# Kernel tuning notes

Measured on AMD Instinct MI355X. Metric: run time of the kernel, lower is better.

The kernel has to match this reference:

```python
import jax, jax.numpy as jnp
import numpy as np

B, N, C = 8, 1024, 768
NH, HD = 12, 64  # num_heads, head_dim
S = 32           # spatial_size (H = W = S, N = S*S)


def _rel_pos_idx(h, w):
    # Standard Swin-style relative position index, shape (h*w, h*w)
    coords = np.stack(np.meshgrid(np.arange(h), np.arange(w), indexing='ij'))  # (2, h, w)
    coords = coords.reshape(2, -1)                                             # (2, N)
    rel = coords[:, :, None] - coords[:, None, :]                              # (2, N, N)
    rel = rel.transpose(1, 2, 0).astype(np.int64)                              # (N, N, 2)
    rel[:, :, 0] += h - 1
    rel[:, :, 1] += w - 1
    rel[:, :, 0] *= 2 * w - 1
    return rel.sum(-1).astype(np.int32)                                        # (N, N)


def setup_inputs() -> dict:
    key = jax.random.key(0)
    ks = jax.random.split(key, 7)
    lim = (1.0 / C) ** 0.5
    x = jax.random.normal(ks[0], (B, N, C), dtype=jnp.float32)
    Wq = jax.random.uniform(ks[1], (C, C), minval=-lim, maxval=lim, dtype=jnp.float32)
    bq = jax.random.uniform(ks[2], (C,), minval=-lim, maxval=lim, dtype=jnp.float32)
    Wkv = jax.random.uniform(ks[3], (2 * C, C), minval=-lim, maxval=lim, dtype=jnp.float32)
    bkv = jax.random.uniform(ks[4], (2 * C,), minval=-lim, maxval=lim, dtype=jnp.float32)
    rel_bias = jax.random.uniform(ks[5], ((2 * S - 1) * (2 * S - 1), NH), dtype=jnp.float32)
    rel_idx = jnp.asarray(_rel_pos_idx(S, S))  # (N, N) int32
    return {"x": x, "Wq": Wq, "bq": bq, "Wkv": Wkv, "bkv": bkv,
            "rel_bias": rel_bias, "rel_idx": rel_idx, "H": S, "W": S}


def reference(x, Wq, bq, Wkv, bkv, rel_bias, rel_idx, H, W):
    b, n, c = x.shape
    scale = HD ** (-0.5)
    # Q projection: (B, NH, N, HD)
    q = (x @ Wq.T + bq).reshape(b, n, NH, HD).transpose(0, 2, 1, 3) * scale
    # KV projection (reduction_factor == 1, no downsample)
    kv = (x @ Wkv.T + bkv).reshape(b, n, 2, NH, HD)
    k = kv[:, :, 0].transpose(0, 2, 1, 3)  # (B, NH, N, HD)
    v = kv[:, :, 1].transpose(0, 2, 1, 3)  # (B, NH, N, HD)
    # Attention scores + gathered relative-position bias
    attn = jnp.einsum('bhqd,bhkd->bhqk', q, k)
    bias = rel_bias[rel_idx]                # (N, N, NH) gather
    attn = attn + bias.transpose(2, 0, 1)[None]
    attn = jax.nn.softmax(attn, axis=-1)
    out = jnp.einsum('bhqk,bhkd->bhqd', attn, v)
    out = out.transpose(0, 2, 1, 3).reshape(b, n, c)
    # NOTE: original forward never applies self.proj; dropout p=0 is identity.
    return out
```

## Files before the change

### kernel.cpp

```cpp
#include <hip/hip_runtime.h>


using bf16x8 = __attribute__((ext_vector_type(8))) short;
using f32x4  = __attribute__((ext_vector_type(4))) float;
using s16x4  = __attribute__((ext_vector_type(4))) short;
using f32x4v = __attribute__((ext_vector_type(4))) float;

#define DEVINL __device__ __forceinline__

#if __has_builtin(__builtin_amdgcn_exp2f)
#define EXP2(x) __builtin_amdgcn_exp2f(x)
#else
#define EXP2(x) __expf((x) * 0.6931471805599453f)
#endif

DEVINL float b2f(short s) {
  union { unsigned u; float f; } v;
  v.u = ((unsigned)(unsigned short)s) << 16;
  return v.f;
}
DEVINL short f2b(float f) {
  union { float f; unsigned u; } v; v.f = f;
  unsigned r = v.u + 0x7fffu + ((v.u >> 16) & 1u);
  return (short)(r >> 16);
}

DEVINL int is_bf16(const unsigned* xraw) {
  int cnt = 0;
#pragma unroll
  for (int i = 0; i < 64; ++i) {
    unsigned e = (xraw[i] >> 7) & 0xffu;
    cnt += (e >= 0x60u && e <= 0xa0u) ? 1 : 0;
  }
  return cnt >= 48;
}

DEVINL void gl_lds16(const short* g, short* l) {
  __builtin_amdgcn_global_load_lds(
      (const __attribute__((address_space(1))) unsigned int*)g,
      (__attribute__((address_space(3))) unsigned int*)l, 16, 0, 0);
}

__global__ __launch_bounds__(256) void convert_kernel(
    const void* __restrict__ x, const void* __restrict__ wq,
    const void* __restrict__ bq, const void* __restrict__ wkv,
    const void* __restrict__ bkv, const void* __restrict__ rb,
    short* __restrict__ xc, short* __restrict__ wqc, short* __restrict__ bqc,
    short* __restrict__ wkvc, short* __restrict__ bkvc,
    short* __restrict__ rbc) {
  const int bf = is_bf16((const unsigned*)x);
  long t = ((long)blockIdx.x * 256 + threadIdx.x) * 4;
  const void* src; short* dst; long i;
  if (t < 6291456L)      { src = x;   dst = xc;   i = t; }
  else if (t < 6881280L) { src = wq;  dst = wqc;  i = t - 6291456L; }
  else if (t < 6882048L) { src = bq;  dst = bqc;  i = t - 6881280L; }
  else if (t < 8061696L) { src = wkv; dst = wkvc; i = t - 6882048L; }
  else if (t < 8063232L) { src = bkv; dst = bkvc; i = t - 8061696L; }
  else if (t < 8110860L) { src = rb;  dst = rbc;  i = t - 8063232L; }
  else return;
  s16x4 o;
  if (bf) {
    o = *(const s16x4*)((const short*)src + i);
  } else {
    f32x4v v = *(const f32x4v*)((const float*)src + i);
    o[0] = f2b(v[0]); o[1] = f2b(v[1]); o[2] = f2b(v[2]); o[3] = f2b(v[3]);
  }
  *(s16x4*)(dst + i) = o;
}

__global__ __launch_bounds__(256) void bias_pack_kernel(
    const int* __restrict__ rel_idx, const short* __restrict__ rel_bias,
    short* __restrict__ bias_pk) {
  int t = blockIdx.x * 256 + threadIdx.x;
  int l15 = t & 15, qq = (t >> 4) & 255, kt4 = (t >> 12) & 3, kt = t >> 14;
  int k = kt * 64 + kt4 * 16 + l15;
  union { unsigned long long u[3]; short s[12]; } row[4];
#pragma unroll
  for (int r = 0; r < 4; ++r) {
    int q = qq * 4 + r;
    int idx = rel_idx[q * 1024 + k];
    const unsigned long long* src =
        (const unsigned long long*)(rel_bias + (size_t)idx * 12);
    row[r].u[0] = src[0]; row[r].u[1] = src[1]; row[r].u[2] = src[2];
  }
#pragma unroll
  for (int hh = 0; hh < 12; ++hh) {
    s16x4 v;
    v[0] = f2b(b2f(row[0].s[hh]) * 1.44269504f);
    v[1] = f2b(b2f(row[1].s[hh]) * 1.44269504f);
    v[2] = f2b(b2f(row[2].s[hh]) * 1.44269504f);
    v[3] = f2b(b2f(row[3].s[hh]) * 1.44269504f);
    *(s16x4*)(bias_pk +
              ((((size_t)(hh * 16 + kt) * 4 + kt4) * 256 + qq) * 16 + l15) * 4) = v;
  }
}

__global__ __launch_bounds__(512, 6) void qkv_gemm_kernel(
    const short* __restrict__ x, const short* __restrict__ wq,
    const short* __restrict__ wkv, const short* __restrict__ bq,
    const short* __restrict__ bkv, short* __restrict__ qbuf,
    short* __restrict__ kbuf, short* __restrict__ vtbuf) {
  __shared__ short lds_a[8192];
  __shared__ short lds_b[8192];
  const int tid = threadIdx.x;
  const int w = tid >> 6, lane = tid & 63, quad = lane >> 4, l15 = lane & 15;
  const int bid = blockIdx.x;
  const int xcd = bid & 7, local = bid >> 3;
  const int m_tile = xcd * 8 + (local & 7), n_tile = local >> 3;
  const int m0 = m_tile * 128, n0 = n_tile * 128;
  const short* wsrc = (n0 < 768) ? (wq + (size_t)n0 * 768)
                                 : (wkv + (size_t)(n0 - 768) * 768);
  const int wm = (w & 1) * 64, wn = (w >> 1) * 32;
  const int lrow = lane >> 3;
  const int lcol = ((lane & 7) ^ lrow) * 8;
  f32x4 acc[4][2] = {};

  for (int k0 = 0; k0 < 768; k0 += 64) {
    __syncthreads();
#pragma unroll
    for (int c = 0; c < 2; ++c) {
      int r0 = (c * 8 + w) * 8;
      gl_lds16(x + (size_t)(m0 + r0 + lrow) * 768 + k0 + lcol, &lds_a[r0 * 64]);
      gl_lds16(wsrc + (size_t)(r0 + lrow) * 768 + k0 + lcol, &lds_b[r0 * 64]);
    }
    __syncthreads();
#pragma unroll
    for (int ks = 0; ks < 2; ++ks) {
      bf16x8 af[4], bg[2];
#pragma unroll
      for (int i = 0; i < 4; ++i) {
        int row = wm + i * 16 + l15;
        af[i] = *(const bf16x8*)
            &lds_a[row * 64 + (((ks * 4 + quad) ^ (row & 7)) * 8)];
      }
#pragma unroll
      for (int j = 0; j < 2; ++j) {
        int row = wn + j * 16 + l15;
        bg[j] = *(const bf16x8*)
            &lds_b[row * 64 + (((ks * 4 + quad) ^ (row & 7)) * 8)];
      }
#pragma unroll
      for (int i = 0; i < 4; ++i)
#pragma unroll
        for (int j = 0; j < 2; ++j)
          acc[i][j] = __builtin_amdgcn_mfma_f32_16x16x32_bf16(af[i], bg[j],
                                                              acc[i][j], 0, 0, 0);
    }
  }

  float biasv[2];
#pragma unroll
  for (int j = 0; j < 2; ++j) {
    int ncol = n0 + wn + j * 16 + l15;
    biasv[j] = b2f(ncol < 768 ? bq[ncol] : bkv[ncol - 768]);
  }
#pragma unroll
  for (int i = 0; i < 4; ++i)
#pragma unroll
    for (int r = 0; r < 4; ++r) {
      int m = m0 + wm + i * 16 + quad * 4 + r;
      int bb = m >> 10, nrow = m & 1023;
#pragma unroll
      for (int j = 0; j < 2; ++j) {
        int ncol = n0 + wn + j * 16 + l15;
        float v = acc[i][j][r] + biasv[j];
        if (n0 < 768) {
          int hh = ncol >> 6, d = ncol & 63;
          qbuf[(((size_t)bb * 12 + hh) * 1024 + nrow) * 64 + d] =
              f2b(v * 0.18033688f);
        } else if (n0 < 1536) {
          int c2 = ncol - 768, hh = c2 >> 6, d = c2 & 63;
          kbuf[(((size_t)bb * 12 + hh) * 1024 + nrow) * 64 + d] = f2b(v);
        } else {
          int c2 = ncol - 1536, hh = c2 >> 6, d = c2 & 63;
          vtbuf[(((size_t)bb * 12 + hh) * 64 + d) * 1024 + nrow] = f2b(v);
        }
      }
    }
}

__global__ __launch_bounds__(256) void attn_kernel(
    const short* __restrict__ qbuf, const short* __restrict__ kbuf,
    const short* __restrict__ vtbuf, const short* __restrict__ bias_pk,
    const void* __restrict__ xraw, void* __restrict__ out) {
  __shared__ short lds_k[64 * 72];
  __shared__ short lds_v[64 * 72];
  __shared__ short lds_p[64 * 40];
  const int tid = threadIdx.x;
  const int w = tid >> 6, lane = tid & 63, quad = lane >> 4, l15 = lane & 15;
  const int qt = blockIdx.y, bh = blockIdx.x;
  const int b = bh / 12, h = bh - b * 12;
  const short* kbase = kbuf + (size_t)bh * 65536;
  const short* vbase = vtbuf + (size_t)bh * 65536;
  short* ldsp_w = &lds_p[w * 16 * 40];

  bf16x8 qf[2];
#pragma unroll
  for (int ks = 0; ks < 2; ++ks)
    qf[ks] = *(const bf16x8*)(qbuf +
        ((size_t)(bh * 1024 + qt * 64 + w * 16 + l15) * 64 + ks * 32 + quad * 8));

  bf16x8 ones;
#pragma unroll
  for (int z = 0; z < 8; ++z) ones[z] = (short)0x3F80;

  f32x4 acc_o[4] = {};
  f32x4 acc_l = {};
  const int srow = tid >> 3, sc = tid & 7;
  const int qq = qt * 16 + w * 4 + quad;

  bf16x8 rk[2], rv[2];
#pragma unroll
  for (int p = 0; p < 2; ++p) {
    int rr = p * 32 + srow;
    rk[p] = *(const bf16x8*)(kbase + (size_t)rr * 64 + sc * 8);
    rv[p] = *(const bf16x8*)(vbase + (size_t)rr * 1024 + sc * 8);
  }

  for (int kt = 0; kt < 16; ++kt) {
    __syncthreads();
#pragma unroll
    for (int p = 0; p < 2; ++p) {
      int rr = p * 32 + srow;
      *(bf16x8*)&lds_k[rr * 72 + sc * 8] = rk[p];
      *(bf16x8*)&lds_v[rr * 72 + sc * 8] = rv[p];
    }
    __syncthreads();
    if (kt < 15) {
#pragma unroll
      for (int p = 0; p < 2; ++p) {
        int rr = p * 32 + srow;
        rk[p] = *(const bf16x8*)(kbase + (size_t)((kt + 1) * 64 + rr) * 64 + sc * 8);
        rv[p] = *(const bf16x8*)(vbase + (size_t)rr * 1024 + (kt + 1) * 64 + sc * 8);
      }
    }

    f32x4 s[4];
#pragma unroll
    for (int c = 0; c < 4; ++c) {
      s16x4 bv = *(const s16x4*)(bias_pk +
          ((((size_t)(h * 16 + kt) * 4 + c) * 256 + qq) * 16 + l15) * 4);
#pragma unroll
      for (int r = 0; r < 4; ++r) s[c][r] = b2f(bv[r]);
    }
#pragma unroll
    for (int ks = 0; ks < 2; ++ks) {
      bf16x8 bk[4];
#pragma unroll
      for (int c = 0; c < 4; ++c)
        bk[c] = *(const bf16x8*)&lds_k[(c * 16 + l15) * 72 + ks * 32 + quad * 8];
#pragma unroll
      for (int c = 0; c < 4; ++c)
        s[c] = __builtin_amdgcn_mfma_f32_16x16x32_bf16(qf[ks], bk[c],
                                                       s[c], 0, 0, 0);
    }
#pragma unroll
    for (int ks = 0; ks < 2; ++ks) {
#pragma unroll
      for (int cl = 0; cl < 2; ++cl) {
        int c = ks * 2 + cl;
#pragma unroll
        for (int r = 0; r < 4; ++r)
          ldsp_w[(quad * 4 + r) * 40 + cl * 16 + l15] = f2b(EXP2(s[c][r]));
      }
      bf16x8 ap = *(const bf16x8*)&ldsp_w[l15 * 40 + quad * 8];
      acc_l = __builtin_amdgcn_mfma_f32_16x16x32_bf16(ap, ones, acc_l, 0, 0, 0);
      bf16x8 bv[4];
#pragma unroll
      for (int dt = 0; dt < 4; ++dt)
        bv[dt] = *(const bf16x8*)&lds_v[(dt * 16 + l15) * 72 + ks * 32 + quad * 8];
#pragma unroll
      for (int dt = 0; dt < 4; ++dt)
        acc_o[dt] = __builtin_amdgcn_mfma_f32_16x16x32_bf16(ap, bv[dt],
                                                            acc_o[dt], 0, 0, 0);
    }
  }
  const int bf = is_bf16((const unsigned*)xraw);
  short* outb = (short*)out;
  float* outf = (float*)out;
#pragma unroll
  for (int r = 0; r < 4; ++r) {
    float inv = 1.0f / fmaxf(acc_l[r], 1e-35f);
    int q = qt * 64 + w * 16 + quad * 4 + r;
    size_t o0 = ((size_t)b * 1024 + q) * 768 + h * 64;
    if (bf) {
#pragma unroll
      for (int dt = 0; dt < 4; ++dt)
        outb[o0 + dt * 16 + l15] = f2b(acc_o[dt][r] * inv);
    } else {
#pragma unroll
      for (int dt = 0; dt < 4; ++dt)
        outf[o0 + dt * 16 + l15] = acc_o[dt][r] * inv;
    }
  }
}

extern "C" void kernel_launch(void* const* d_in, const int* in_sizes, int n_in,
                              void* d_out, int out_size, void* d_ws, size_t ws_size,
                              hipStream_t stream) {
  const void* x        = d_in[0];
  const void* wq       = d_in[1];
  const void* bq       = d_in[2];
  const void* wkv      = d_in[3];
  const void* bkv      = d_in[4];
  const void* rel_bias = d_in[5];
  const int*  rel_idx  = (const int*)d_in[6];

  char* ws = (char*)d_ws;
  short* qbuf    = (short*)(ws);
  short* kbuf    = (short*)(ws + 12582912);
  short* vtbuf   = (short*)(ws + 25165824);
  short* bias_pk = (short*)(ws + 37748736);
  short* xc      = (short*)(ws + 62914560);
  short* wqc     = (short*)(ws + 75497472);
  short* bqc     = (short*)(ws + 76677120);
  short* wkvc    = (short*)(ws + 76678656);
  short* bkvc    = (short*)(ws + 79037952);
  short* rbc     = (short*)(ws + 79041024);

  convert_kernel<<<7921, 256, 0, stream>>>(x, wq, bq, wkv, bkv, rel_bias,
                                           xc, wqc, bqc, wkvc, bkvc, rbc);
  bias_pack_kernel<<<1024, 256, 0, stream>>>(rel_idx, rbc, bias_pk);
  qkv_gemm_kernel<<<1152, 512, 0, stream>>>(xc, wqc, wkvc, bqc, bkvc,
                                            qbuf, kbuf, vtbuf);
  attn_kernel<<<dim3(96, 16), 256, 0, stream>>>(qbuf, kbuf, vtbuf, bias_pk,
                                                x, (void*)d_out);
}
```

Before: 215.3 us.

## Switch attention to 32x32x16 MFMA with register-resident P via permlane swap

```diff
diff --git a/kernel.cpp b/kernel.cpp
--- a/kernel.cpp
+++ b/kernel.cpp
@@ -3,6 +3,7 @@
 
 using bf16x8 = __attribute__((ext_vector_type(8))) short;
 using f32x4  = __attribute__((ext_vector_type(4))) float;
+using f32x16 = __attribute__((ext_vector_type(16))) float;
 using s16x4  = __attribute__((ext_vector_type(4))) short;
 using f32x4v = __attribute__((ext_vector_type(4))) float;
 
@@ -23,6 +24,15 @@
   union { float f; unsigned u; } v; v.f = f;
   unsigned r = v.u + 0x7fffu + ((v.u >> 16) & 1u);
   return (short)(r >> 16);
+}
+
+DEVINL unsigned cvtpk(float lo, float hi) {
+  unsigned r;
+  asm("v_cvt_pk_bf16_f32 %0, %1, %2" : "=v"(r) : "v"(lo), "v"(hi));
+  return r;
+}
+DEVINL void plswap(unsigned& a, unsigned& b) {
+  asm("v_permlane32_swap_b32 %0, %1" : "+v"(a), "+v"(b));
 }
 
 DEVINL int is_bf16(const unsigned* xraw) {
@@ -72,12 +82,11 @@
     const int* __restrict__ rel_idx, const short* __restrict__ rel_bias,
     short* __restrict__ bias_pk) {
   int t = blockIdx.x * 256 + threadIdx.x;
-  int l15 = t & 15, qq = (t >> 4) & 255, kt4 = (t >> 12) & 3, kt = t >> 14;
-  int k = kt * 64 + kt4 * 16 + l15;
-  union { unsigned long long u[3]; short s[12]; } row[4];
-#pragma unroll
-  for (int r = 0; r < 4; ++r) {
-    int q = qq * 4 + r;
+  int hi = t & 1, q = (t >> 1) & 1023, kt2 = t >> 11;
+  union { unsigned long long u[3]; short s[12]; } row[16];
+#pragma unroll
+  for (int r = 0; r < 16; ++r) {
+    int k = kt2 * 32 + (r & 3) + 8 * (r >> 2) + 4 * hi;
     int idx = rel_idx[q * 1024 + k];
     const unsigned long long* src =
         (const unsigned long long*)(rel_bias + (size_t)idx * 12);
@@ -85,13 +94,13 @@
   }
 #pragma unroll
   for (int hh = 0; hh < 12; ++hh) {
-    s16x4 v;
-    v[0] = f2b(b2f(row[0].s[hh]) * 1.44269504f);
-    v[1] = f2b(b2f(row[1].s[hh]) * 1.44269504f);
-    v[2] = f2b(b2f(row[2].s[hh]) * 1.44269504f);
-    v[3] = f2b(b2f(row[3].s[hh]) * 1.44269504f);
-    *(s16x4*)(bias_pk +
-              ((((size_t)(hh * 16 + kt) * 4 + kt4) * 256 + qq) * 16 + l15) * 4) = v;
+    union { short s[16]; bf16x8 v[2]; } o;
+#pragma unroll
+    for (int r = 0; r < 16; ++r)
+      o.s[r] = f2b(b2f(row[r].s[hh]) * 1.44269504f);
+    short* dst = bias_pk + ((((size_t)hh * 32 + kt2) * 1024 + q) * 2 + hi) * 16;
+    *(bf16x8*)dst = o.v[0];
+    *(bf16x8*)(dst + 8) = o.v[1];
   }
 }
 
@@ -179,35 +188,34 @@
     }
 }
 
-__global__ __launch_bounds__(256) void attn_kernel(
+__global__ __launch_bounds__(256, 3) void attn_kernel(
     const short* __restrict__ qbuf, const short* __restrict__ kbuf,
     const short* __restrict__ vtbuf, const short* __restrict__ bias_pk,
     const void* __restrict__ xraw, void* __restrict__ out) {
-  __shared__ short lds_k[64 * 72];
-  __shared__ short lds_v[64 * 72];
-  __shared__ short lds_p[64 * 40];
+  __shared__ short lds_k[64 * 64];
+  __shared__ short lds_v[64 * 64];
   const int tid = threadIdx.x;
-  const int w = tid >> 6, lane = tid & 63, quad = lane >> 4, l15 = lane & 15;
+  const int w = tid >> 6, lane = tid & 63, l31 = lane & 31, hi = lane >> 5;
   const int qt = blockIdx.y, bh = blockIdx.x;
   const int b = bh / 12, h = bh - b * 12;
   const short* kbase = kbuf + (size_t)bh * 65536;
   const short* vbase = vtbuf + (size_t)bh * 65536;
-  short* ldsp_w = &lds_p[w * 16 * 40];
-
-  bf16x8 qf[2];
-#pragma unroll
-  for (int ks = 0; ks < 2; ++ks)
-    qf[ks] = *(const bf16x8*)(qbuf +
-        ((size_t)(bh * 1024 + qt * 64 + w * 16 + l15) * 64 + ks * 32 + quad * 8));
+  const int q0 = qt * 128 + w * 32;
+
+  bf16x8 qf[4];
+#pragma unroll
+  for (int ds = 0; ds < 4; ++ds)
+    qf[ds] = *(const bf16x8*)(qbuf +
+        ((size_t)(bh * 1024 + q0 + l31) * 64 + ds * 16 + hi * 8));
 
   bf16x8 ones;
 #pragma unroll
   for (int z = 0; z < 8; ++z) ones[z] = (short)0x3F80;
 
-  f32x4 acc_o[4] = {};
-  f32x4 acc_l = {};
+  f32x16 acc_o[2] = {};
+  f32x16 acc_l = {};
+
   const int srow = tid >> 3, sc = tid & 7;
-  const int qq = qt * 16 + w * 4 + quad;
 
   bf16x8 rk[2], rv[2];
 #pragma unroll
@@ -217,80 +225,95 @@
     rv[p] = *(const bf16x8*)(vbase + (size_t)rr * 1024 + sc * 8);
   }
 
+  const short* bias_base =
+      bias_pk + (((size_t)h * 32 * 1024 + q0 + l31) * 2 + hi) * 16;
+
   for (int kt = 0; kt < 16; ++kt) {
     __syncthreads();
 #pragma unroll
     for (int p = 0; p < 2; ++p) {
       int rr = p * 32 + srow;
-      *(bf16x8*)&lds_k[rr * 72 + sc * 8] = rk[p];
-      *(bf16x8*)&lds_v[rr * 72 + sc * 8] = rv[p];
+      int wa = rr * 64 + ((sc ^ (rr & 7)) * 8);
+      *(bf16x8*)&lds_k[wa] = rk[p];
+      *(bf16x8*)&lds_v[wa] = rv[p];
     }
     __syncthreads();
     if (kt < 15) {
 #pragma unroll
       for (int p = 0; p < 2; ++p) {
         int rr = p * 32 + srow;
-        rk[p] = *(const bf16x8*)(kbase + (size_t)((kt + 1) * 64 + rr) * 64 + sc * 8);
-        rv[p] = *(const bf16x8*)(vbase + (size_t)rr * 1024 + (kt + 1) * 64 + sc * 8);
-      }
-    }
-
-    f32x4 s[4];
-#pragma unroll
-    for (int c = 0; c < 4; ++c) {
-      s16x4 bv = *(const s16x4*)(bias_pk +
-          ((((size_t)(h * 16 + kt) * 4 + c) * 256 + qq) * 16 + l15) * 4);
-#pragma unroll
-      for (int r = 0; r < 4; ++r) s[c][r] = b2f(bv[r]);
-    }
-#pragma unroll
-    for (int ks = 0; ks < 2; ++ks) {
-      bf16x8 bk[4];
-#pragma unroll
-      for (int c = 0; c < 4; ++c)
-        bk[c] = *(const bf16x8*)&lds_k[(c * 16 + l15) * 72 + ks * 32 + quad * 8];
-#pragma unroll
-      for (int c = 0; c < 4; ++c)
-        s[c] = __builtin_amdgcn_mfma_f32_16x16x32_bf16(qf[ks], bk[c],
-                                                       s[c], 0, 0, 0);
-    }
-#pragma unroll
-    for (int ks = 0; ks < 2; ++ks) {
-#pragma unroll
-      for (int cl = 0; cl < 2; ++cl) {
-        int c = ks * 2 + cl;
-#pragma unroll
-        for (int r = 0; r < 4; ++r)
-          ldsp_w[(quad * 4 + r) * 40 + cl * 16 + l15] = f2b(EXP2(s[c][r]));
-      }
-      bf16x8 ap = *(const bf16x8*)&ldsp_w[l15 * 40 + quad * 8];
-      acc_l = __builtin_amdgcn_mfma_f32_16x16x32_bf16(ap, ones, acc_l, 0, 0, 0);
-      bf16x8 bv[4];
-#pragma unroll
-      for (int dt = 0; dt < 4; ++dt)
-        bv[dt] = *(const bf16x8*)&lds_v[(dt * 16 + l15) * 72 + ks * 32 + quad * 8];
-#pragma unroll
-      for (int dt = 0; dt < 4; ++dt)
-        acc_o[dt] = __builtin_amdgcn_mfma_f32_16x16x32_bf16(ap, bv[dt],
-                                                            acc_o[dt], 0, 0, 0);
-    }
-  }
-  const int bf = is_bf16((const unsigned*)xraw);
+        rk[p] = *(const bf16x8*)(kbase +
+                  (size_t)((kt + 1) * 64 + rr) * 64 + sc * 8);
+        rv[p] = *(const bf16x8*)(vbase +
+                  (size_t)rr * 1024 + (kt + 1) * 64 + sc * 8);
+      }
+    }
+
+#pragma unroll
+    for (int st = 0; st < 2; ++st) {
+      const short* bb = bias_base + (size_t)(kt * 2 + st) * (1024 * 2 * 16);
+      bf16x8 bv0 = *(const bf16x8*)bb;
+      bf16x8 bv1 = *(const bf16x8*)(bb + 8);
+      f32x16 s;
+#pragma unroll
+      for (int r = 0; r < 8; ++r) s[r] = b2f(bv0[r]);
+#pragma unroll
+      for (int r = 0; r < 8; ++r) s[8 + r] = b2f(bv1[r]);
+#pragma unroll
+      for (int ds = 0; ds < 4; ++ds) {
+        int krow = st * 32 + l31;
+        bf16x8 kf = *(const bf16x8*)
+            &lds_k[krow * 64 + (((ds * 2 + hi) ^ (krow & 7)) * 8)];
+        s = __builtin_amdgcn_mfma_f32_32x32x16_bf16(kf, qf[ds], s, 0, 0, 0);
+      }
+      float p[16];
+#pragma unroll
+      for (int r = 0; r < 16; ++r) p[r] = EXP2(s[r]);
+#pragma unroll
+      for (int kk = 0; kk < 2; ++kk) {
+        unsigned wa = cvtpk(p[kk * 8 + 0], p[kk * 8 + 1]);
+        unsigned wb = cvtpk(p[kk * 8 + 4], p[kk * 8 + 5]);
+        unsigned wc = cvtpk(p[kk * 8 + 2], p[kk * 8 + 3]);
+        unsigned wd = cvtpk(p[kk * 8 + 6], p[kk * 8 + 7]);
+        plswap(wa, wb);
+        plswap(wc, wd);
+        union { unsigned u[4]; bf16x8 v; } pa;
+        pa.u[0] = wa; pa.u[1] = wc; pa.u[2] = wb; pa.u[3] = wd;
+        acc_l = __builtin_amdgcn_mfma_f32_32x32x16_bf16(pa.v, ones, acc_l,
+                                                        0, 0, 0);
+#pragma unroll
+        for (int dt = 0; dt < 2; ++dt) {
+          int vd = dt * 32 + l31;
+          bf16x8 vf = *(const bf16x8*)
+              &lds_v[vd * 64 + (((st * 4 + kk * 2 + hi) ^ (vd & 7)) * 8)];
+          acc_o[dt] = __builtin_amdgcn_mfma_f32_32x32x16_bf16(pa.v, vf,
+                                                              acc_o[dt],
+                                                              0, 0, 0);
+        }
+      }
+    }
+  }
+
+  const int bfo = is_bf16((const unsigned*)xraw);
   short* outb = (short*)out;
   float* outf = (float*)out;
-#pragma unroll
-  for (int r = 0; r < 4; ++r) {
-    float inv = 1.0f / fmaxf(acc_l[r], 1e-35f);
-    int q = qt * 64 + w * 16 + quad * 4 + r;
-    size_t o0 = ((size_t)b * 1024 + q) * 768 + h * 64;
-    if (bf) {
-#pragma unroll
-      for (int dt = 0; dt < 4; ++dt)
-        outb[o0 + dt * 16 + l15] = f2b(acc_o[dt][r] * inv);
-    } else {
-#pragma unroll
-      for (int dt = 0; dt < 4; ++dt)
-        outf[o0 + dt * 16 + l15] = acc_o[dt][r] * inv;
+  if (bfo) {
+#pragma unroll
+    for (int r = 0; r < 16; ++r) {
+      float inv = 1.0f / fmaxf(acc_l[r], 1e-35f);
+      int q = qt * 128 + w * 32 + (r & 3) + 8 * (r >> 2) + 4 * hi;
+      size_t o0 = ((size_t)b * 1024 + q) * 768 + h * 64 + l31;
+      outb[o0] = f2b(acc_o[0][r] * inv);
+      outb[o0 + 32] = f2b(acc_o[1][r] * inv);
+    }
+  } else {
+#pragma unroll
+    for (int r = 0; r < 16; ++r) {
+      float inv = 1.0f / fmaxf(acc_l[r], 1e-35f);
+      int q = qt * 128 + w * 32 + (r & 3) + 8 * (r >> 2) + 4 * hi;
+      size_t o0 = ((size_t)b * 1024 + q) * 768 + h * 64 + l31;
+      outf[o0] = acc_o[0][r] * inv;
+      outf[o0 + 32] = acc_o[1][r] * inv;
     }
   }
 }
@@ -320,9 +343,9 @@
 
   convert_kernel<<<7921, 256, 0, stream>>>(x, wq, bq, wkv, bkv, rel_bias,
                                            xc, wqc, bqc, wkvc, bkvc, rbc);
-  bias_pack_kernel<<<1024, 256, 0, stream>>>(rel_idx, rbc, bias_pk);
+  bias_pack_kernel<<<256, 256, 0, stream>>>(rel_idx, rbc, bias_pk);
   qkv_gemm_kernel<<<1152, 512, 0, stream>>>(xc, wqc, wkvc, bqc, bkvc,
                                             qbuf, kbuf, vtbuf);
-  attn_kernel<<<dim3(96, 16), 256, 0, stream>>>(qbuf, kbuf, vtbuf, bias_pk,
-                                                x, (void*)d_out);
-}
+  attn_kernel<<<dim3(96, 8), 256, 0, stream>>>(qbuf, kbuf, vtbuf, bias_pk,
+                                               x, (void*)d_out);
+}
```

Result: faster. 199.0 us (median of 2 runs) (-7.6%).
